# Kernel tuning notes

Measured on AMD Instinct MI355X. Metric: run time of the kernel, lower is better.

## Reference

```python
import jax, jax.numpy as jnp
import numpy as np

C = 128          # channel_size
H = 2            # num_head
HD = C // H      # per-head dim = 64
SCALE = C ** 0.5 # note: module scales by sqrt(channel_size), not sqrt(head_dim)


def setup_inputs() -> dict:
    key = jax.random.key(0)
    k_x, k_w, k_b = jax.random.split(key, 3)
    x = jax.random.normal(k_x, (8, 64, 256, C), dtype=jnp.float32)
    # nn.Linear(C, 3C): weight [3C, C], bias [3C]; y = x @ W.T + b
    bound = 1.0 / np.sqrt(C)
    W_qkv = jax.random.uniform(k_w, (3 * C, C), dtype=jnp.float32, minval=-bound, maxval=bound)
    b_qkv = jax.random.uniform(k_b, (3 * C,), dtype=jnp.float32, minval=-bound, maxval=bound)
    return {"x": x, "W_qkv": W_qkv, "b_qkv": b_qkv}


def reference(x, W_qkv, b_qkv):
    b, l, g, _ = x.shape
    qkv = jnp.einsum('blgc,dc->blgd', x, W_qkv) + b_qkv        # [b,l,g,3C]
    # rearrange 'b l g (d h c) -> d b l h g c'
    qkv = qkv.reshape(b, l, g, 3, H, HD)
    qkv = jnp.transpose(qkv, (3, 0, 1, 4, 2, 5))               # [3,b,l,h,g,c]
    q, k, v = qkv[0], qkv[1], qkv[2]
    score = jnp.einsum('blhgc,blhkc->blhgk', q, k) / SCALE      # [b,l,h,g,g]
    score = jax.nn.softmax(score, axis=-1)
    out = jnp.einsum('blhgk,blhkc->blhgc', score, v)            # [b,l,h,g,c]
    # rearrange 'b l h g c -> b l g (h c)'
    out = jnp.transpose(out, (0, 1, 3, 2, 4)).reshape(b, l, g, H * HD)
    return out
```

## Files before the change

kernel.cpp:

```cpp
#include <hip/hip_runtime.h>
#include <hip/hip_bf16.h>


typedef __bf16 bf16x8 __attribute__((ext_vector_type(8)));
typedef float  f32x4  __attribute__((ext_vector_type(4)));
typedef float  f32x16 __attribute__((ext_vector_type(16)));

#define MFMA16(a, b, c) __builtin_amdgcn_mfma_f32_16x16x32_bf16((a), (b), (c), 0, 0, 0)
#define MFMA32(a, b, c) __builtin_amdgcn_mfma_f32_32x32x16_bf16((a), (b), (c), 0, 0, 0)

namespace dmsa {

constexpr int G  = 256;
constexpr int C  = 128;
constexpr int HD = 64;
constexpr float QSCALE = 1.4426950408889634f * 0.08838834764831845f;

__device__ __forceinline__ unsigned pack2(float a, float b) {
    union { __hip_bfloat162 h; unsigned u; } c;
    c.h = __float22bfloat162_rn(make_float2(a, b));
    return c.u;
}
__device__ __forceinline__ uint2 pack4(float a, float b, float c, float d) {
    uint2 r; r.x = pack2(a, b); r.y = pack2(c, d); return r;
}
__device__ __forceinline__ uint4 pack8(const float* p) {
    uint4 r;
    r.x = pack2(p[0], p[1]); r.y = pack2(p[2], p[3]);
    r.z = pack2(p[4], p[5]); r.w = pack2(p[6], p[7]);
    return r;
}
__device__ __forceinline__ bf16x8 lds8(const ushort* p) { return *(const bf16x8*)p; }
__device__ __forceinline__ bf16x8 ldg8(const ushort* p) { return *(const bf16x8*)p; }
__device__ __forceinline__ bf16x8 ld8f(const float* __restrict__ p) {
    float t[8];
    *(float4*)t       = *(const float4*)p;
    *(float4*)(t + 4) = *(const float4*)(p + 4);
    union { uint4 u; bf16x8 v; } c;
    c.u = pack8(t);
    return c.v;
}

__global__ void convw(const float* __restrict__ W, ushort* __restrict__ wbf) {
    int t = blockIdx.x * 256 + threadIdx.x;
    float tmp[8];
    const float* p = W + (size_t)t * 8;
    *(float4*)tmp       = *(const float4*)p;
    *(float4*)(tmp + 4) = *(const float4*)(p + 4);
    *(uint4*)(wbf + (size_t)t * 8) = pack8(tmp);
}

__global__ __launch_bounds__(256, 2)
void fused(const float* __restrict__ x, const ushort* __restrict__ wb,
           const float* __restrict__ bias, float* __restrict__ out)
{
    __shared__ ushort kc[G * 72];
    __shared__ ushort vc[HD * 264];

    const int tid = threadIdx.x, wv = tid >> 6, lane = tid & 63;
    const int l16 = lane & 15, quad = lane >> 4;
    const int l32 = lane & 31, hl = lane >> 5;

    const int b  = blockIdx.x;
    const int L  = ((b & 7) << 7) | (b >> 3);
    const int bl = L >> 1, h = L & 1;

    const float*  xr = x  + (size_t)bl * G * C;
    const ushort* Wq = wb + (size_t)(h * HD) * C;
    const ushort* Wk = wb + (size_t)(C + h * HD) * C;
    const ushort* Wv = wb + (size_t)(2 * C + h * HD) * C;

    const int r0 = wv * 64;
    const f32x4 z4 = {0.f, 0.f, 0.f, 0.f};

    bf16x8 xf[4][4];
    #pragma unroll
    for (int i = 0; i < 4; ++i)
        #pragma unroll
        for (int kk = 0; kk < 4; ++kk)
            xf[i][kk] = ld8f(xr + (size_t)(r0 + i * 16 + l16) * C + kk * 32 + quad * 8);

    f32x4 qacc[4][4];
    #pragma unroll
    for (int mi = 0; mi < 4; ++mi)
        #pragma unroll
        for (int ni = 0; ni < 4; ++ni) qacc[mi][ni] = z4;
    #pragma unroll
    for (int kk = 0; kk < 4; ++kk)
        #pragma unroll
        for (int mi = 0; mi < 4; ++mi) {
            bf16x8 a = ldg8(Wq + (size_t)(mi * 16 + l16) * C + kk * 32 + quad * 8);
            #pragma unroll
            for (int ni = 0; ni < 4; ++ni)
                qacc[mi][ni] = MFMA16(a, xf[ni][kk], qacc[mi][ni]);
        }
    ushort* qs = kc + r0 * 72;
    #pragma unroll
    for (int mi = 0; mi < 4; ++mi) {
        float4 bs = *(const float4*)(bias + h * HD + mi * 16 + quad * 4);
        #pragma unroll
        for (int ni = 0; ni < 4; ++ni)
            *(uint2*)(qs + (ni * 16 + l16) * 72 + mi * 16 + quad * 4) =
                pack4((qacc[mi][ni][0] + bs.x) * QSCALE,
                      (qacc[mi][ni][1] + bs.y) * QSCALE,
                      (qacc[mi][ni][2] + bs.z) * QSCALE,
                      (qacc[mi][ni][3] + bs.w) * QSCALE);
    }
    bf16x8 qf[2][4];
    #pragma unroll
    for (int ni = 0; ni < 2; ++ni)
        #pragma unroll
        for (int kk = 0; kk < 4; ++kk)
            qf[ni][kk] = lds8(qs + (ni * 32 + l32) * 72 + kk * 16 + hl * 8);

    {
        f32x4 kacc[4][4];
        #pragma unroll
        for (int mi = 0; mi < 4; ++mi)
            #pragma unroll
            for (int nt = 0; nt < 4; ++nt) kacc[mi][nt] = z4;
        #pragma unroll
        for (int kk = 0; kk < 4; ++kk)
            #pragma unroll
            for (int mi = 0; mi < 4; ++mi) {
                bf16x8 a = ldg8(Wk + (size_t)(mi * 16 + l16) * C + kk * 32 + quad * 8);
                #pragma unroll
                for (int nt = 0; nt < 4; ++nt)
                    kacc[mi][nt] = MFMA16(a, xf[nt][kk], kacc[mi][nt]);
            }
        #pragma unroll
        for (int mi = 0; mi < 4; ++mi) {
            float4 bs = *(const float4*)(bias + C + h * HD + mi * 16 + quad * 4);
            #pragma unroll
            for (int nt = 0; nt < 4; ++nt)
                *(uint2*)(kc + (r0 + nt * 16 + l16) * 72 + mi * 16 + quad * 4) =
                    pack4(kacc[mi][nt][0] + bs.x, kacc[mi][nt][1] + bs.y,
                          kacc[mi][nt][2] + bs.z, kacc[mi][nt][3] + bs.w);
        }
    }

    {
        f32x4 vacc[4][4];
        #pragma unroll
        for (int mt = 0; mt < 4; ++mt)
            #pragma unroll
            for (int nt = 0; nt < 4; ++nt) vacc[mt][nt] = z4;
        #pragma unroll
        for (int kk = 0; kk < 4; ++kk)
            #pragma unroll
            for (int nt = 0; nt < 4; ++nt) {
                bf16x8 bw = ldg8(Wv + (size_t)(nt * 16 + l16) * C + kk * 32 + quad * 8);
                #pragma unroll
                for (int mt = 0; mt < 4; ++mt)
                    vacc[mt][nt] = MFMA16(xf[mt][kk], bw, vacc[mt][nt]);
            }
        #pragma unroll
        for (int nt = 0; nt < 4; ++nt) {
            float bv = bias[2 * C + h * HD + nt * 16 + l16];
            #pragma unroll
            for (int mt = 0; mt < 4; ++mt)
                *(uint2*)(vc + (nt * 16 + l16) * 264 + r0 + mt * 16 + quad * 4) =
                    pack4(vacc[mt][nt][0] + bv, vacc[mt][nt][1] + bv,
                          vacc[mt][nt][2] + bv, vacc[mt][nt][3] + bv);
        }
    }

    __syncthreads();

    float lacc[2] = {0.f, 0.f};
    f32x16 oacc[2][2];
    #pragma unroll
    for (int mt = 0; mt < 2; ++mt)
        #pragma unroll
        for (int ni = 0; ni < 2; ++ni)
            #pragma unroll
            for (int r = 0; r < 16; ++r) oacc[mt][ni][r] = 0.f;

    #pragma unroll 2
    for (int sp = 0; sp < 8; ++sp) {
        const int g0 = sp * 32;

        bf16x8 kf[4];
        #pragma unroll
        for (int kk = 0; kk < 4; ++kk)
            kf[kk] = lds8(kc + (g0 + l32) * 72 + kk * 16 + hl * 8);
        bf16x8 vf[2][2];
        #pragma unroll
        for (int mt = 0; mt < 2; ++mt)
            #pragma unroll
            for (int ch = 0; ch < 2; ++ch)
                vf[mt][ch] = lds8(vc + (mt * 32 + l32) * 264 + g0 + ch * 16 + hl * 8);

        #pragma unroll
        for (int ni = 0; ni < 2; ++ni) {
            f32x16 s;
            #pragma unroll
            for (int r = 0; r < 16; ++r) s[r] = 0.f;
            __builtin_amdgcn_s_setprio(1);
            #pragma unroll
            for (int kk = 0; kk < 4; ++kk)
                s = MFMA32(kf[kk], qf[ni][kk], s);
            __builtin_amdgcn_s_setprio(0);

            float part = 0.f;
            #pragma unroll
            for (int r = 0; r < 16; ++r) {
                float p = exp2f(s[r]);
                s[r] = p;
                part += p;
            }
            lacc[ni] += part;

            #pragma unroll
            for (int ch = 0; ch < 2; ++ch) {
                unsigned p0a = pack2(s[8 * ch + 0], s[8 * ch + 1]);
                unsigned p0b = pack2(s[8 * ch + 2], s[8 * ch + 3]);
                unsigned p1a = pack2(s[8 * ch + 4], s[8 * ch + 5]);
                unsigned p1b = pack2(s[8 * ch + 6], s[8 * ch + 7]);
                auto w02 = __builtin_amdgcn_permlane32_swap((int)p0a, (int)p1a, false, false);
                auto w13 = __builtin_amdgcn_permlane32_swap((int)p0b, (int)p1b, false, false);
                union { uint4 u; bf16x8 v; } pf;
                pf.u.x = (unsigned)w02[0]; pf.u.y = (unsigned)w13[0];
                pf.u.z = (unsigned)w02[1]; pf.u.w = (unsigned)w13[1];
                __builtin_amdgcn_s_setprio(1);
                #pragma unroll
                for (int mt = 0; mt < 2; ++mt)
                    oacc[mt][ni] = MFMA32(vf[mt][ch], pf.v, oacc[mt][ni]);
                __builtin_amdgcn_s_setprio(0);
            }
        }
    }

    float* og = out + (size_t)bl * G * C + h * HD;
    #pragma unroll
    for (int ni = 0; ni < 2; ++ni) {
        float l = lacc[ni];
        l += __shfl_xor(l, 32);
        float inv = 1.0f / l;
        int g = r0 + ni * 32 + l32;
        #pragma unroll
        for (int mt = 0; mt < 2; ++mt)
            #pragma unroll
            for (int rr = 0; rr < 4; ++rr) {
                float4 st;
                st.x = oacc[mt][ni][4 * rr + 0] * inv;
                st.y = oacc[mt][ni][4 * rr + 1] * inv;
                st.z = oacc[mt][ni][4 * rr + 2] * inv;
                st.w = oacc[mt][ni][4 * rr + 3] * inv;
                *(float4*)(og + (size_t)g * C + mt * 32 + rr * 8 + hl * 4) = st;
            }
    }
}

}

extern "C" void kernel_launch(void* const* d_in, const int* in_sizes, int n_in,
                              void* d_out, int out_size, void* d_ws, size_t ws_size,
                              hipStream_t stream) {
    (void)in_sizes; (void)n_in; (void)out_size;

    if (ws_size < (size_t)384 * 128 * 2) return;

    const float* x    = (const float*)d_in[0];
    const float* W    = (const float*)d_in[1];
    const float* bias = (const float*)d_in[2];
    float* out = (float*)d_out;

    ushort* wbf = (ushort*)d_ws;

    dmsa::convw<<<dim3(24),   dim3(256), 0, stream>>>(W, wbf);
    dmsa::fused<<<dim3(1024), dim3(256), 0, stream>>>(x, wbf, bias, out);
}
```

Baseline: 166.1 us.

## Drop weight-conversion kernel, widen attention tile, and stagger LDS access

Removes the separate fp32-to-bf16 weight conversion launch; the fused kernel now reads fp32 weights and converts them inline. The attention loop processes 64 keys per step, batching all QK MFMAs, then exp/pack, then all PV MFMAs, and rotates each wave's starting key block to spread LDS bank traffic. It also uses fast exp2/rcp intrinsics and a tree sum. This saves a launch and increases MFMA batching, at the cost of doubled weight-load bytes per block, redundant conversion work, and higher register pressure.

```diff
diff --git a/kernel.cpp b/kernel.cpp
--- a/kernel.cpp
+++ b/kernel.cpp
@@ -31,7 +31,6 @@
     return r;
 }
 __device__ __forceinline__ bf16x8 lds8(const ushort* p) { return *(const bf16x8*)p; }
-__device__ __forceinline__ bf16x8 ldg8(const ushort* p) { return *(const bf16x8*)p; }
 __device__ __forceinline__ bf16x8 ld8f(const float* __restrict__ p) {
     float t[8];
     *(float4*)t       = *(const float4*)p;
@@ -41,17 +40,8 @@
     return c.v;
 }
 
-__global__ void convw(const float* __restrict__ W, ushort* __restrict__ wbf) {
-    int t = blockIdx.x * 256 + threadIdx.x;
-    float tmp[8];
-    const float* p = W + (size_t)t * 8;
-    *(float4*)tmp       = *(const float4*)p;
-    *(float4*)(tmp + 4) = *(const float4*)(p + 4);
-    *(uint4*)(wbf + (size_t)t * 8) = pack8(tmp);
-}
-
 __global__ __launch_bounds__(256, 2)
-void fused(const float* __restrict__ x, const ushort* __restrict__ wb,
+void fused(const float* __restrict__ x, const float* __restrict__ W,
            const float* __restrict__ bias, float* __restrict__ out)
 {
     __shared__ ushort kc[G * 72];
@@ -65,10 +55,10 @@
     const int L  = ((b & 7) << 7) | (b >> 3);
     const int bl = L >> 1, h = L & 1;
 
-    const float*  xr = x  + (size_t)bl * G * C;
-    const ushort* Wq = wb + (size_t)(h * HD) * C;
-    const ushort* Wk = wb + (size_t)(C + h * HD) * C;
-    const ushort* Wv = wb + (size_t)(2 * C + h * HD) * C;
+    const float* xr = x + (size_t)bl * G * C;
+    const float* Wq = W + (size_t)(h * HD) * C;
+    const float* Wk = W + (size_t)(C + h * HD) * C;
+    const float* Wv = W + (size_t)(2 * C + h * HD) * C;
 
     const int r0 = wv * 64;
     const f32x4 z4 = {0.f, 0.f, 0.f, 0.f};
@@ -89,7 +79,7 @@
     for (int kk = 0; kk < 4; ++kk)
         #pragma unroll
         for (int mi = 0; mi < 4; ++mi) {
-            bf16x8 a = ldg8(Wq + (size_t)(mi * 16 + l16) * C + kk * 32 + quad * 8);
+            bf16x8 a = ld8f(Wq + (size_t)(mi * 16 + l16) * C + kk * 32 + quad * 8);
             #pragma unroll
             for (int ni = 0; ni < 4; ++ni)
                 qacc[mi][ni] = MFMA16(a, xf[ni][kk], qacc[mi][ni]);
@@ -123,7 +113,7 @@
         for (int kk = 0; kk < 4; ++kk)
             #pragma unroll
             for (int mi = 0; mi < 4; ++mi) {
-                bf16x8 a = ldg8(Wk + (size_t)(mi * 16 + l16) * C + kk * 32 + quad * 8);
+                bf16x8 a = ld8f(Wk + (size_t)(mi * 16 + l16) * C + kk * 32 + quad * 8);
                 #pragma unroll
                 for (int nt = 0; nt < 4; ++nt)
                     kacc[mi][nt] = MFMA16(a, xf[nt][kk], kacc[mi][nt]);
@@ -149,7 +139,7 @@
         for (int kk = 0; kk < 4; ++kk)
             #pragma unroll
             for (int nt = 0; nt < 4; ++nt) {
-                bf16x8 bw = ldg8(Wv + (size_t)(nt * 16 + l16) * C + kk * 32 + quad * 8);
+                bf16x8 bw = ld8f(Wv + (size_t)(nt * 16 + l16) * C + kk * 32 + quad * 8);
                 #pragma unroll
                 for (int mt = 0; mt < 4; ++mt)
                     vacc[mt][nt] = MFMA16(xf[mt][kk], bw, vacc[mt][nt]);
@@ -176,59 +166,82 @@
             #pragma unroll
             for (int r = 0; r < 16; ++r) oacc[mt][ni][r] = 0.f;
 
+    const int spoff = (wv + ((b & 1) << 1)) & 3;
+
     #pragma unroll 2
-    for (int sp = 0; sp < 8; ++sp) {
-        const int g0 = sp * 32;
-
-        bf16x8 kf[4];
-        #pragma unroll
-        for (int kk = 0; kk < 4; ++kk)
-            kf[kk] = lds8(kc + (g0 + l32) * 72 + kk * 16 + hl * 8);
-        bf16x8 vf[2][2];
+    for (int sp = 0; sp < 4; ++sp) {
+        const int g0 = ((sp + spoff) & 3) * 64;
+
+        bf16x8 kf[2][4];
+        #pragma unroll
+        for (int mi = 0; mi < 2; ++mi)
+            #pragma unroll
+            for (int kk = 0; kk < 4; ++kk)
+                kf[mi][kk] = lds8(kc + (g0 + mi * 32 + l32) * 72 + kk * 16 + hl * 8);
+        bf16x8 vf[2][4];
         #pragma unroll
         for (int mt = 0; mt < 2; ++mt)
             #pragma unroll
-            for (int ch = 0; ch < 2; ++ch)
-                vf[mt][ch] = lds8(vc + (mt * 32 + l32) * 264 + g0 + ch * 16 + hl * 8);
-
+            for (int cc = 0; cc < 4; ++cc)
+                vf[mt][cc] = lds8(vc + (mt * 32 + l32) * 264 + g0 + cc * 16 + hl * 8);
+
+        f32x16 s[2][2];
+        #pragma unroll
+        for (int mi = 0; mi < 2; ++mi)
+            #pragma unroll
+            for (int ni = 0; ni < 2; ++ni)
+                #pragma unroll
+                for (int r = 0; r < 16; ++r) s[mi][ni][r] = 0.f;
+        __builtin_amdgcn_s_setprio(1);
+        #pragma unroll
+        for (int kk = 0; kk < 4; ++kk)
+            #pragma unroll
+            for (int mi = 0; mi < 2; ++mi)
+                #pragma unroll
+                for (int ni = 0; ni < 2; ++ni)
+                    s[mi][ni] = MFMA32(kf[mi][kk], qf[ni][kk], s[mi][ni]);
+        __builtin_amdgcn_s_setprio(0);
+
+        bf16x8 pfr[2][4];
         #pragma unroll
         for (int ni = 0; ni < 2; ++ni) {
-            f32x16 s;
-            #pragma unroll
-            for (int r = 0; r < 16; ++r) s[r] = 0.f;
-            __builtin_amdgcn_s_setprio(1);
-            #pragma unroll
-            for (int kk = 0; kk < 4; ++kk)
-                s = MFMA32(kf[kk], qf[ni][kk], s);
-            __builtin_amdgcn_s_setprio(0);
-
             float part = 0.f;
             #pragma unroll
-            for (int r = 0; r < 16; ++r) {
-                float p = exp2f(s[r]);
-                s[r] = p;
-                part += p;
+            for (int mi = 0; mi < 2; ++mi) {
+                f32x16& sv = s[mi][ni];
+                #pragma unroll
+                for (int r = 0; r < 16; ++r) sv[r] = __builtin_amdgcn_exp2f(sv[r]);
+                float a0 = (sv[0] + sv[1]) + (sv[2] + sv[3]);
+                float a1 = (sv[4] + sv[5]) + (sv[6] + sv[7]);
+                float a2 = (sv[8] + sv[9]) + (sv[10] + sv[11]);
+                float a3 = (sv[12] + sv[13]) + (sv[14] + sv[15]);
+                part += (a0 + a1) + (a2 + a3);
+                #pragma unroll
+                for (int ch = 0; ch < 2; ++ch) {
+                    unsigned p0a = pack2(sv[8 * ch + 0], sv[8 * ch + 1]);
+                    unsigned p0b = pack2(sv[8 * ch + 2], sv[8 * ch + 3]);
+                    unsigned p1a = pack2(sv[8 * ch + 4], sv[8 * ch + 5]);
+                    unsigned p1b = pack2(sv[8 * ch + 6], sv[8 * ch + 7]);
+                    auto w02 = __builtin_amdgcn_permlane32_swap((int)p0a, (int)p1a, false, false);
+                    auto w13 = __builtin_amdgcn_permlane32_swap((int)p0b, (int)p1b, false, false);
+                    union { uint4 u; bf16x8 v; } pf_;
+                    pf_.u.x = (unsigned)w02[0]; pf_.u.y = (unsigned)w13[0];
+                    pf_.u.z = (unsigned)w02[1]; pf_.u.w = (unsigned)w13[1];
+                    pfr[ni][mi * 2 + ch] = pf_.v;
+                }
             }
             lacc[ni] += part;
-
-            #pragma unroll
-            for (int ch = 0; ch < 2; ++ch) {
-                unsigned p0a = pack2(s[8 * ch + 0], s[8 * ch + 1]);
-                unsigned p0b = pack2(s[8 * ch + 2], s[8 * ch + 3]);
-                unsigned p1a = pack2(s[8 * ch + 4], s[8 * ch + 5]);
-                unsigned p1b = pack2(s[8 * ch + 6], s[8 * ch + 7]);
-                auto w02 = __builtin_amdgcn_permlane32_swap((int)p0a, (int)p1a, false, false);
-                auto w13 = __builtin_amdgcn_permlane32_swap((int)p0b, (int)p1b, false, false);
-                union { uint4 u; bf16x8 v; } pf;
-                pf.u.x = (unsigned)w02[0]; pf.u.y = (unsigned)w13[0];
-                pf.u.z = (unsigned)w02[1]; pf.u.w = (unsigned)w13[1];
-                __builtin_amdgcn_s_setprio(1);
-                #pragma unroll
-                for (int mt = 0; mt < 2; ++mt)
-                    oacc[mt][ni] = MFMA32(vf[mt][ch], pf.v, oacc[mt][ni]);
-                __builtin_amdgcn_s_setprio(0);
-            }
-        }
+        }
+
+        __builtin_amdgcn_s_setprio(1);
+        #pragma unroll
+        for (int cc = 0; cc < 4; ++cc)
+            #pragma unroll
+            for (int mt = 0; mt < 2; ++mt)
+                #pragma unroll
+                for (int ni = 0; ni < 2; ++ni)
+                    oacc[mt][ni] = MFMA32(vf[mt][cc], pfr[ni][cc], oacc[mt][ni]);
+        __builtin_amdgcn_s_setprio(0);
     }
 
     float* og = out + (size_t)bl * G * C + h * HD;
@@ -236,7 +249,7 @@
     for (int ni = 0; ni < 2; ++ni) {
         float l = lacc[ni];
         l += __shfl_xor(l, 32);
-        float inv = 1.0f / l;
+        float inv = __builtin_amdgcn_rcpf(l);
         int g = r0 + ni * 32 + l32;
         #pragma unroll
         for (int mt = 0; mt < 2; ++mt)
@@ -257,17 +270,12 @@
 extern "C" void kernel_launch(void* const* d_in, const int* in_sizes, int n_in,
                               void* d_out, int out_size, void* d_ws, size_t ws_size,
                               hipStream_t stream) {
-    (void)in_sizes; (void)n_in; (void)out_size;
-
-    if (ws_size < (size_t)384 * 128 * 2) return;
+    (void)in_sizes; (void)n_in; (void)out_size; (void)d_ws; (void)ws_size;
 
     const float* x    = (const float*)d_in[0];
     const float* W    = (const float*)d_in[1];
     const float* bias = (const float*)d_in[2];
     float* out = (float*)d_out;
 
-    ushort* wbf = (ushort*)d_ws;
-
-    dmsa::convw<<<dim3(24),   dim3(256), 0, stream>>>(W, wbf);
-    dmsa::fused<<<dim3(1024), dim3(256), 0, stream>>>(x, wbf, bias, out);
-}
+    dmsa::fused<<<dim3(1024), dim3(256), 0, stream>>>(x, W, bias, out);
+}
```

New measurement: 177.2 us. 6.7% more time.
